# Kernel tuning notes

Measured on AMD Instinct MI355X. Metric: run time of the kernel, lower is better.

Reference implementation:

```python
import jax, jax.numpy as jnp
import numpy as np

N, E, D, H, C = 50000, 1600000, 128, 2, 32

def setup_inputs() -> dict:
    key = jax.random.key(0)
    ks = jax.random.split(key, 8)
    x = jax.random.normal(ks[0], (N, D), jnp.float32)
    edge_index = jax.random.randint(ks[1], (2, E), 0, N)
    intra_enrichment_weights = jax.random.uniform(ks[2], (E,), jnp.float32)
    W = jax.random.normal(ks[3], (D, H * C), jnp.float32) * (1.0 / np.sqrt(D))
    att_src = jax.random.normal(ks[4], (H, C), jnp.float32) * 0.1
    att_dst = jax.random.normal(ks[5], (H, C), jnp.float32) * 0.1
    bias = jnp.zeros((H * C,), jnp.float32)
    enrichment_scale = jnp.asarray(0.01, jnp.float32)
    return dict(x=x, edge_index=edge_index,
                intra_enrichment_weights=intra_enrichment_weights,
                W=W, att_src=att_src, att_dst=att_dst, bias=bias,
                enrichment_scale=enrichment_scale)

def reference(x, edge_index, intra_enrichment_weights, W, att_src, att_dst, bias, enrichment_scale):
    n = x.shape[0]
    xf = jax.nn.elu(x)                       # F.elu on input features
    h = (xf @ W).reshape(n, H, C)            # [N, heads, out]
    # GATConv default add_self_loops=True
    loop = jnp.arange(n, dtype=edge_index.dtype)
    src = jnp.concatenate([edge_index[0], loop])
    dst = jnp.concatenate([edge_index[1], loop])
    a_src = jnp.einsum('nhc,hc->nh', h, att_src)   # [N, H]
    a_dst = jnp.einsum('nhc,hc->nh', h, att_dst)
    alpha = jax.nn.leaky_relu(a_src[src] + a_dst[dst], 0.2)  # [E+N, H]
    # softmax over incoming edges per destination node
    m = jax.ops.segment_max(alpha, dst, num_segments=n)
    e = jnp.exp(alpha - m[dst])
    denom = jax.ops.segment_sum(e, dst, num_segments=n)
    p = e / denom[dst]                       # every node has a self-loop -> denom > 0
    out = jax.ops.segment_sum(h[src] * p[:, :, None], dst, num_segments=n)  # [N, H, C]
    out = out.reshape(n, H * C) + bias
    # enrichment bias (scatter-mean of per-edge weights over source nodes)
    s0 = edge_index[0]
    nw = jax.ops.segment_sum(intra_enrichment_weights, s0, num_segments=n)
    cnt = jax.ops.segment_sum(jnp.ones_like(intra_enrichment_weights), s0, num_segments=n)
    nw = nw / jnp.maximum(cnt, 1.0)
    nw = jnp.clip(nw, 0.2, 5.0)
    scale_factor = 0.1 * jax.nn.sigmoid(enrichment_scale)
    return out + scale_factor * (nw[:, None] - 1.0)
```

## Files before the change

kernel.cpp:

```cpp
#include <hip/hip_runtime.h>


typedef unsigned int u32;
typedef unsigned short u16;

#define SLOTS 4864
#define NB_MAX 400
#define EPB 4096

#define XS 136
#define CS 68

typedef __attribute__((ext_vector_type(8))) short short8;
typedef __attribute__((ext_vector_type(4))) float float4v;

__device__ __forceinline__ u16 f2bf(float f) {
    union { float f; u32 u; } v; v.f = f;
    u32 r = v.u + 0x7fffu + ((v.u >> 16) & 1u);
    return (u16)(r >> 16);
}
__device__ __forceinline__ float bf2f(u16 u) {
    union { u32 i; float f; } v; v.i = ((u32)u) << 16; return v.f;
}
__device__ __forceinline__ float bf_lo(u32 u) {
    union { u32 i; float f; } v; v.i = u << 16; return v.f;
}
__device__ __forceinline__ float bf_hi(u32 u) {
    union { u32 i; float f; } v; v.i = u & 0xFFFF0000u; return v.f;
}
__device__ __forceinline__ void bf_split(float v, short& hi, short& lo) {
    u16 h = f2bf(v);
    float hf = bf2f(h);
    hi = (short)h;
    lo = (short)f2bf(v - hf);
}

__global__ void k_prep(const float* __restrict__ Wm,
                       short* __restrict__ Whf, short* __restrict__ Wlf,
                       int* cursA, int* cursB)
{
    int t = threadIdx.x;
    for (int i = t; i < NB_MAX; i += 256) { cursA[i] = 0; cursB[i] = 0; }
    for (int p = t; p < 1024; p += 256) {
        int frag = p >> 6, l = p & 63;
        int ks = frag >> 2, nt = frag & 3;
        int q = l >> 4, m = l & 15;
        int f = nt * 16 + m;
#pragma unroll
        for (int j = 0; j < 8; ++j) {
            int k = ks * 32 + q * 8 + j;
            float wv = Wm[k * 64 + f];
            short hi, lo; bf_split(wv, hi, lo);
            Whf[p * 8 + j] = hi;
            Wlf[p * 8 + j] = lo;
        }
    }
}

__global__ __launch_bounds__(256) void k_node(
    const float* __restrict__ x,
    const short* __restrict__ Whf, const short* __restrict__ Wlf,
    const float* __restrict__ att_s, const float* __restrict__ att_d,
    u32* __restrict__ hb32, float* __restrict__ a_src, float* __restrict__ a_dst,
    int nN)
{
    __shared__ __align__(16) short Ah[64 * XS];
    __shared__ __align__(16) short Al[64 * XS];
    float* Cl = (float*)Ah;

    int t = threadIdx.x;
    int n0 = blockIdx.x * 64;

    for (int j = 0; j < 8; ++j) {
        int idx = t + 256 * j;
        int r = idx >> 5, c4 = idx & 31;
        int gn = n0 + r;
        float4 xv = make_float4(0.f, 0.f, 0.f, 0.f);
        if (gn < nN) xv = ((const float4*)x)[(size_t)gn * 32 + c4];
        float e[4];
        e[0] = xv.x > 0.f ? xv.x : __expf(xv.x) - 1.f;
        e[1] = xv.y > 0.f ? xv.y : __expf(xv.y) - 1.f;
        e[2] = xv.z > 0.f ? xv.z : __expf(xv.z) - 1.f;
        e[3] = xv.w > 0.f ? xv.w : __expf(xv.w) - 1.f;
        short h4[4], l4[4];
#pragma unroll
        for (int i = 0; i < 4; ++i) bf_split(e[i], h4[i], l4[i]);
        *(short4*)&Ah[r * XS + c4 * 4] = make_short4(h4[0], h4[1], h4[2], h4[3]);
        *(short4*)&Al[r * XS + c4 * 4] = make_short4(l4[0], l4[1], l4[2], l4[3]);
    }
    __syncthreads();

    {
        int w = t >> 6, l = t & 63;
        int q = l >> 4, m = l & 15;
        int arow = w * 16 + m;
        float4v acc[4] = {};
#pragma unroll
        for (int ks = 0; ks < 4; ++ks) {
            int k0 = ks * 32 + q * 8;
            short8 ah = *(const short8*)&Ah[arow * XS + k0];
            short8 al = *(const short8*)&Al[arow * XS + k0];
#pragma unroll
            for (int nt = 0; nt < 4; ++nt) {
                short8 bh = *(const short8*)&Whf[((ks * 4 + nt) * 64 + l) * 8];
                short8 bl = *(const short8*)&Wlf[((ks * 4 + nt) * 64 + l) * 8];
                acc[nt] = __builtin_amdgcn_mfma_f32_16x16x32_bf16(ah, bh, acc[nt], 0, 0, 0);
                acc[nt] = __builtin_amdgcn_mfma_f32_16x16x32_bf16(ah, bl, acc[nt], 0, 0, 0);
                acc[nt] = __builtin_amdgcn_mfma_f32_16x16x32_bf16(al, bh, acc[nt], 0, 0, 0);
            }
        }
        __syncthreads();
#pragma unroll
        for (int nt = 0; nt < 4; ++nt)
#pragma unroll
            for (int r = 0; r < 4; ++r)
                Cl[(w * 16 + q * 4 + r) * CS + nt * 16 + m] = acc[nt][r];
    }
    __syncthreads();

    {
        int nl = t >> 2, fq = t & 3;
        int gn = n0 + nl;
        float ps = 0.f, pd = 0.f;
        if (gn < nN) {
            float hv[16];
#pragma unroll
            for (int i = 0; i < 16; ++i) {
                int f = fq * 16 + i;
                hv[i] = Cl[nl * CS + f];
                ps = fmaf(hv[i], att_s[f], ps);
                pd = fmaf(hv[i], att_d[f], pd);
            }
#pragma unroll
            for (int i = 0; i < 8; ++i) {
                u32 pk = ((u32)f2bf(hv[2 * i + 1]) << 16) | (u32)f2bf(hv[2 * i]);
                hb32[(size_t)gn * 32 + fq * 8 + i] = pk;
            }
        }
        float ps2 = ps + __shfl_xor(ps, 1, 64);
        float pd2 = pd + __shfl_xor(pd, 1, 64);
        if (gn < nN && (fq & 1) == 0) {
            a_src[2 * gn + (fq >> 1)] = ps2;
            a_dst[2 * gn + (fq >> 1)] = pd2;
        }
    }
}

__global__ __launch_bounds__(256) void k_partA(
    const int* __restrict__ ei, const float* __restrict__ wgt,
    int* cursA, int* cursB, u32* bufA, u32* bufB, int E, int nb)
{
    __shared__ u32 arrA[EPB], arrB[EPB];
    __shared__ int cntA[NB_MAX], cntB[NB_MAX];
    __shared__ int lofsA[NB_MAX], lofsB[NB_MAX];
    __shared__ int basA[NB_MAX], basB[NB_MAX];
    __shared__ int part[256];

    int t = threadIdx.x;
    for (int b = t; b < nb; b += 256) { cntA[b] = 0; cntB[b] = 0; }
    __syncthreads();

    int base = blockIdx.x * EPB;
    int nv = min(EPB, E - base);
    int sv[16], dv[16]; float wv[16];
#pragma unroll
    for (int k = 0; k < 16; ++k) {
        int e = base + k * 256 + t;
        if (e < E) { sv[k] = ei[e]; dv[k] = ei[E + e]; wv[k] = wgt[e]; }
        else       { sv[k] = -1;    dv[k] = -1;        wv[k] = 0.f; }
    }
#pragma unroll
    for (int k = 0; k < 16; ++k) {
        if (dv[k] >= 0) {
            atomicAdd(&cntA[dv[k] >> 7], 1);
            atomicAdd(&cntB[sv[k] >> 7], 1);
        }
    }
    __syncthreads();
    for (int b = t; b < nb; b += 256) {
        int ca = cntA[b], cb = cntB[b];
        if (ca > 0) basA[b] = atomicAdd(&cursA[b], ca);
        if (cb > 0) basB[b] = atomicAdd(&cursB[b], cb);
    }
    __syncthreads();
    {
        int b0 = 2 * t, b1 = 2 * t + 1;
        int c0 = (b0 < nb) ? cntA[b0] : 0;
        int c1 = (b1 < nb) ? cntA[b1] : 0;
        part[t] = c0 + c1;
        __syncthreads();
        for (int off = 1; off < 256; off <<= 1) {
            int v = (t >= off) ? part[t - off] : 0;
            __syncthreads();
            part[t] += v;
            __syncthreads();
        }
        int excl = part[t] - (c0 + c1);
        if (b0 < nb) lofsA[b0] = excl;
        if (b1 < nb) lofsA[b1] = excl + c0;
        __syncthreads();
        c0 = (b0 < nb) ? cntB[b0] : 0;
        c1 = (b1 < nb) ? cntB[b1] : 0;
        part[t] = c0 + c1;
        __syncthreads();
        for (int off = 1; off < 256; off <<= 1) {
            int v = (t >= off) ? part[t - off] : 0;
            __syncthreads();
            part[t] += v;
            __syncthreads();
        }
        excl = part[t] - (c0 + c1);
        if (b0 < nb) lofsB[b0] = excl;
        if (b1 < nb) lofsB[b1] = excl + c0;
    }
    __syncthreads();
    for (int b = t; b < nb; b += 256) { cntA[b] = 0; cntB[b] = 0; }
    __syncthreads();
#pragma unroll
    for (int k = 0; k < 16; ++k) {
        if (dv[k] >= 0) {
            int bA = dv[k] >> 7;
            int r = lofsA[bA] + atomicAdd(&cntA[bA], 1);
            arrA[r] = ((u32)bA << 23) | ((u32)(dv[k] & 127) << 16) | (u32)sv[k];
            int bB = sv[k] >> 7;
            u32 wf = (u32)(wv[k] * 65536.f);
            if (wf > 0xFFFFu) wf = 0xFFFFu;
            int r2 = lofsB[bB] + atomicAdd(&cntB[bB], 1);
            arrB[r2] = ((u32)sv[k] << 16) | wf;
        }
    }
    __syncthreads();
    for (int i = t; i < nv; i += 256) {
        u32 va = arrA[i];
        int bA = va >> 23;
        int g = basA[bA] + (i - lofsA[bA]);
        if (g < SLOTS) bufA[bA * SLOTS + g] = va & 0x7FFFFFu;
        u32 vb = arrB[i];
        int bB = vb >> 23;
        int g2 = basB[bB] + (i - lofsB[bB]);
        if (g2 < SLOTS) bufB[bB * SLOTS + g2] = vb & 0x7FFFFFu;
    }
}

__global__ __launch_bounds__(1024) void k_final(
    const u32* __restrict__ hb32,
    const float* __restrict__ a_src, const float* __restrict__ a_dst,
    const u32* __restrict__ bufA, const int* __restrict__ cursA,
    const u32* __restrict__ bufB, const int* __restrict__ cursB,
    const float* __restrict__ bias, const float* __restrict__ esc,
    float* __restrict__ out, int nN)
{
    __shared__ u32 st[SLOTS];
    __shared__ u16 st2[SLOTS];
    __shared__ int ldeg[128], lscan[128], lcur[128];
    __shared__ u32 usum[128];
    __shared__ int ucnt[128];

    int b = blockIdx.x, t = threadIdx.x;
    int n0 = b << 7;
    int nA = cursA[b]; if (nA > SLOTS) nA = SLOTS;
    int nB = cursB[b]; if (nB > SLOTS) nB = SLOTS;

    if (t < 128) { ldeg[t] = 0; lcur[t] = 0; usum[t] = 0; ucnt[t] = 0; }
    __syncthreads();
    for (int i = t; i < nA; i += 1024) {
        u32 v = bufA[(size_t)b * SLOTS + i];
        st[i] = v;
        atomicAdd(&ldeg[v >> 16], 1);
    }
    for (int i = t; i < nB; i += 1024) {
        u32 v = bufB[(size_t)b * SLOTS + i];
        atomicAdd(&usum[v >> 16], v & 0xFFFFu);
        atomicAdd(&ucnt[v >> 16], 1);
    }
    __syncthreads();
    if (t < 128) lscan[t] = ldeg[t];
    __syncthreads();
    for (int off = 1; off < 128; off <<= 1) {
        int v = 0;
        if (t < 128 && t >= off) v = lscan[t - off];
        __syncthreads();
        if (t < 128) lscan[t] += v;
        __syncthreads();
    }
    if (t < 128) lscan[t] -= ldeg[t];
    __syncthreads();
    for (int i = t; i < nA; i += 1024) {
        u32 v = st[i];
        int dl = v >> 16;
        int pos = lscan[dl] + atomicAdd(&lcur[dl], 1);
        st2[pos] = (u16)(v & 0xFFFFu);
    }
    __syncthreads();

    int ws = t >> 6, lane = t & 63;
    int q = lane >> 4, fl = lane & 15, head = fl >> 3;
    const uint2* hb2 = (const uint2*)hb32;
    float escv = esc[0];
    float sf = 0.1f / (1.f + __expf(-escv));
    float4 bb = ((const float4*)bias)[fl];

    for (int dl = ws; dl < 128; dl += 16) {
        int gn = n0 + dl;
        if (gn >= nN) break;
        int beg = lscan[dl], cnt = ldeg[dl];
        float2 adv = ((const float2*)a_dst)[gn];
        float2 asv = ((const float2*)a_src)[gn];
        float t0 = asv.x + adv.x; t0 = t0 > 0.f ? t0 : 0.2f * t0;
        float t1 = asv.y + adv.y; t1 = t1 > 0.f ? t1 : 0.2f * t1;
        float es0 = __expf(t0), es1 = __expf(t1);
        float eself = head ? es1 : es0;

        float acc0 = 0.f, acc1 = 0.f, acc2 = 0.f, acc3 = 0.f;
        if (q == 0) {
            uint2 hs = hb2[(size_t)gn * 16 + fl];
            acc0 = eself * bf_lo(hs.x);
            acc1 = eself * bf_hi(hs.x);
            acc2 = eself * bf_lo(hs.y);
            acc3 = eself * bf_hi(hs.y);
        }
        float dsum0 = 0.f, dsum1 = 0.f;

        int iters = (cnt + 3) >> 2;
#pragma unroll 4
        for (int k = 0; k < iters; ++k) {
            int e = 4 * k + q;
            if (e < cnt) {
                u32 si = st2[beg + e];
                float2 ap = ((const float2*)a_src)[si];
                float v0 = ap.x + adv.x; v0 = v0 > 0.f ? v0 : 0.2f * v0;
                float v1 = ap.y + adv.y; v1 = v1 > 0.f ? v1 : 0.2f * v1;
                float e0 = __expf(v0), e1 = __expf(v1);
                dsum0 += e0; dsum1 += e1;
                uint2 hv = hb2[(size_t)si * 16 + fl];
                float w = head ? e1 : e0;
                acc0 = fmaf(w, bf_lo(hv.x), acc0);
                acc1 = fmaf(w, bf_hi(hv.x), acc1);
                acc2 = fmaf(w, bf_lo(hv.y), acc2);
                acc3 = fmaf(w, bf_hi(hv.y), acc3);
            }
        }
        dsum0 += __shfl_xor(dsum0, 16, 64); dsum0 += __shfl_xor(dsum0, 32, 64);
        dsum1 += __shfl_xor(dsum1, 16, 64); dsum1 += __shfl_xor(dsum1, 32, 64);
        acc0 += __shfl_xor(acc0, 16, 64); acc0 += __shfl_xor(acc0, 32, 64);
        acc1 += __shfl_xor(acc1, 16, 64); acc1 += __shfl_xor(acc1, 32, 64);
        acc2 += __shfl_xor(acc2, 16, 64); acc2 += __shfl_xor(acc2, 32, 64);
        acc3 += __shfl_xor(acc3, 16, 64); acc3 += __shfl_xor(acc3, 32, 64);

        if (q == 0) {
            float den = (head ? es1 : es0) + (head ? dsum1 : dsum0);
            float inv = 1.f / den;
            float cntf = (float)ucnt[dl];
            float nw = ((float)usum[dl] * (1.f / 65536.f)) / fmaxf(cntf, 1.f);
            nw = fminf(fmaxf(nw, 0.2f), 5.f);
            float en = sf * (nw - 1.f);
            float4 o;
            o.x = acc0 * inv + bb.x + en;
            o.y = acc1 * inv + bb.y + en;
            o.z = acc2 * inv + bb.z + en;
            o.w = acc3 * inv + bb.w + en;
            ((float4*)out)[(size_t)gn * 16 + fl] = o;
        }
    }
}

extern "C" void kernel_launch(void* const* d_in, const int* in_sizes, int n_in,
                              void* d_out, int out_size, void* d_ws, size_t ws_size,
                              hipStream_t stream)
{
    const float* x     = (const float*)d_in[0];
    const int*   ei    = (const int*)d_in[1];
    const float* wgt   = (const float*)d_in[2];
    const float* Wm    = (const float*)d_in[3];
    const float* att_s = (const float*)d_in[4];
    const float* att_d = (const float*)d_in[5];
    const float* bias  = (const float*)d_in[6];
    const float* esc   = (const float*)d_in[7];
    float* out = (float*)d_out;

    int nN = in_sizes[0] / 128;
    int E  = in_sizes[2];
    int NB = (nN + 127) / 128;

    char* p = (char*)d_ws;
    auto alloc = [&](size_t bytes) -> char* {
        char* r = p; p += (bytes + 255) & ~(size_t)255; return r;
    };
    u32*   hb32  = (u32*)  alloc((size_t)nN * 32 * 4);
    float* a_src = (float*)alloc((size_t)nN * 2 * 4);
    float* a_dst = (float*)alloc((size_t)nN * 2 * 4);
    short* Whf   = (short*)alloc(16 * 64 * 8 * 2);
    short* Wlf   = (short*)alloc(16 * 64 * 8 * 2);
    int*   cursA = (int*)  alloc(NB_MAX * 4);
    int*   cursB = (int*)  alloc(NB_MAX * 4);
    u32*   bufA  = (u32*)  alloc((size_t)NB * SLOTS * 4);
    u32*   bufB  = (u32*)  alloc((size_t)NB * SLOTS * 4);

    int nblkA = (E + EPB - 1) / EPB;
    int nblkN = (nN + 63) / 64;

    k_prep<<<dim3(1), dim3(256), 0, stream>>>(Wm, Whf, Wlf, cursA, cursB);
    k_node<<<dim3(nblkN), dim3(256), 0, stream>>>(x, Whf, Wlf, att_s, att_d,
                                                  hb32, a_src, a_dst, nN);
    k_partA<<<dim3(nblkA), dim3(256), 0, stream>>>(ei, wgt, cursA, cursB, bufA, bufB, E, NB);
    k_final<<<dim3(NB), dim3(1024), 0, stream>>>(hb32, a_src, a_dst, bufA, cursA,
                                                 bufB, cursB, bias, esc, out, nN);
}
```

Before: 186.7 us.

## Fuse node-transform and edge-partition kernels, lane-parallel edge softmax in final

```diff
diff --git a/kernel.cpp b/kernel.cpp
--- a/kernel.cpp
+++ b/kernel.cpp
@@ -10,6 +10,8 @@
 
 #define XS 136
 #define CS 68
+
+#define SMEM_F 43392
 
 typedef __attribute__((ext_vector_type(8))) short short8;
 typedef __attribute__((ext_vector_type(4))) float float4v;
@@ -57,19 +59,20 @@
     }
 }
 
-__global__ __launch_bounds__(256) void k_node(
+static __device__ __forceinline__ void node_body(
+    char* smem, int nb_id,
     const float* __restrict__ x,
     const short* __restrict__ Whf, const short* __restrict__ Wlf,
     const float* __restrict__ att_s, const float* __restrict__ att_d,
     u32* __restrict__ hb32, float* __restrict__ a_src, float* __restrict__ a_dst,
     int nN)
 {
-    __shared__ __align__(16) short Ah[64 * XS];
-    __shared__ __align__(16) short Al[64 * XS];
+    short* Ah = (short*)smem;
+    short* Al = (short*)(smem + 17408);
     float* Cl = (float*)Ah;
 
     int t = threadIdx.x;
-    int n0 = blockIdx.x * 64;
+    int n0 = nb_id * 64;
 
     for (int j = 0; j < 8; ++j) {
         int idx = t + 256 * j;
@@ -146,21 +149,26 @@
     }
 }
 
-__global__ __launch_bounds__(256) void k_partA(
+static __device__ __forceinline__ void partA_body(
+    char* smem, int pa_id,
     const int* __restrict__ ei, const float* __restrict__ wgt,
     int* cursA, int* cursB, u32* bufA, u32* bufB, int E, int nb)
 {
-    __shared__ u32 arrA[EPB], arrB[EPB];
-    __shared__ int cntA[NB_MAX], cntB[NB_MAX];
-    __shared__ int lofsA[NB_MAX], lofsB[NB_MAX];
-    __shared__ int basA[NB_MAX], basB[NB_MAX];
-    __shared__ int part[256];
+    u32* arrA  = (u32*)smem;
+    u32* arrB  = (u32*)(smem + 16384);
+    int* cntA  = (int*)(smem + 32768);
+    int* cntB  = (int*)(smem + 34368);
+    int* lofsA = (int*)(smem + 35968);
+    int* lofsB = (int*)(smem + 37568);
+    int* basA  = (int*)(smem + 39168);
+    int* basB  = (int*)(smem + 40768);
+    int* part  = (int*)(smem + 42368);
 
     int t = threadIdx.x;
     for (int b = t; b < nb; b += 256) { cntA[b] = 0; cntB[b] = 0; }
     __syncthreads();
 
-    int base = blockIdx.x * EPB;
+    int base = pa_id * EPB;
     int nv = min(EPB, E - base);
     int sv[16], dv[16]; float wv[16];
 #pragma unroll
@@ -226,7 +234,7 @@
             u32 wf = (u32)(wv[k] * 65536.f);
             if (wf > 0xFFFFu) wf = 0xFFFFu;
             int r2 = lofsB[bB] + atomicAdd(&cntB[bB], 1);
-            arrB[r2] = ((u32)sv[k] << 16) | wf;
+            arrB[r2] = ((u32)bB << 23) | ((u32)(sv[k] & 127) << 16) | wf;
         }
     }
     __syncthreads();
@@ -242,6 +250,27 @@
     }
 }
 
+__global__ __launch_bounds__(256) void k_fused(
+    const float* __restrict__ x,
+    const short* __restrict__ Whf, const short* __restrict__ Wlf,
+    const float* __restrict__ att_s, const float* __restrict__ att_d,
+    u32* __restrict__ hb32, float* __restrict__ a_src, float* __restrict__ a_dst,
+    const int* __restrict__ ei, const float* __restrict__ wgt,
+    int* cursA, int* cursB, u32* bufA, u32* bufB,
+    int E, int nb, int nblkA, int nN)
+{
+    __shared__ __align__(16) char smem[SMEM_F];
+    int bid = blockIdx.x;
+    int q3 = bid / 3;
+    if ((bid % 3) == 0 && q3 < nblkA) {
+        partA_body(smem, q3, ei, wgt, cursA, cursB, bufA, bufB, E, nb);
+    } else {
+        int npa_before = min(q3 + ((bid % 3) ? 1 : 0), nblkA);
+        node_body(smem, bid - npa_before, x, Whf, Wlf, att_s, att_d,
+                  hb32, a_src, a_dst, nN);
+    }
+}
+
 __global__ __launch_bounds__(1024) void k_final(
     const u32* __restrict__ hb32,
     const float* __restrict__ a_src, const float* __restrict__ a_dst,
@@ -309,10 +338,10 @@
         float t0 = asv.x + adv.x; t0 = t0 > 0.f ? t0 : 0.2f * t0;
         float t1 = asv.y + adv.y; t1 = t1 > 0.f ? t1 : 0.2f * t1;
         float es0 = __expf(t0), es1 = __expf(t1);
-        float eself = head ? es1 : es0;
 
         float acc0 = 0.f, acc1 = 0.f, acc2 = 0.f, acc3 = 0.f;
         if (q == 0) {
+            float eself = head ? es1 : es0;
             uint2 hs = hb2[(size_t)gn * 16 + fl];
             acc0 = eself * bf_lo(hs.x);
             acc1 = eself * bf_hi(hs.x);
@@ -321,27 +350,38 @@
         }
         float dsum0 = 0.f, dsum1 = 0.f;
 
-        int iters = (cnt + 3) >> 2;
-#pragma unroll 4
-        for (int k = 0; k < iters; ++k) {
-            int e = 4 * k + q;
-            if (e < cnt) {
-                u32 si = st2[beg + e];
+        for (int b0 = 0; b0 < cnt; b0 += 64) {
+            int wn = cnt - b0; if (wn > 64) wn = 64;
+            u32 si = (u32)gn; float e0 = 0.f, e1 = 0.f;
+            if (lane < wn) {
+                si = (u32)st2[beg + b0 + lane];
                 float2 ap = ((const float2*)a_src)[si];
                 float v0 = ap.x + adv.x; v0 = v0 > 0.f ? v0 : 0.2f * v0;
                 float v1 = ap.y + adv.y; v1 = v1 > 0.f ? v1 : 0.2f * v1;
-                float e0 = __expf(v0), e1 = __expf(v1);
-                dsum0 += e0; dsum1 += e1;
-                uint2 hv = hb2[(size_t)si * 16 + fl];
-                float w = head ? e1 : e0;
+                e0 = __expf(v0); e1 = __expf(v1);
+            }
+            dsum0 += e0; dsum1 += e1;
+
+            int iters = (wn + 3) >> 2;
+#pragma unroll 8
+            for (int k = 0; k < iters; ++k) {
+                int e = 4 * k + q;
+                u32 rsi = __shfl(si, e, 64);
+                uint2 hv = hb2[(size_t)rsi * 16 + fl];
+                float w0 = __shfl(e0, e, 64);
+                float w1 = __shfl(e1, e, 64);
+                float w = head ? w1 : w0;
                 acc0 = fmaf(w, bf_lo(hv.x), acc0);
                 acc1 = fmaf(w, bf_hi(hv.x), acc1);
                 acc2 = fmaf(w, bf_lo(hv.y), acc2);
                 acc3 = fmaf(w, bf_hi(hv.y), acc3);
             }
         }
-        dsum0 += __shfl_xor(dsum0, 16, 64); dsum0 += __shfl_xor(dsum0, 32, 64);
-        dsum1 += __shfl_xor(dsum1, 16, 64); dsum1 += __shfl_xor(dsum1, 32, 64);
+#pragma unroll
+        for (int off = 1; off < 64; off <<= 1) {
+            dsum0 += __shfl_xor(dsum0, off, 64);
+            dsum1 += __shfl_xor(dsum1, off, 64);
+        }
         acc0 += __shfl_xor(acc0, 16, 64); acc0 += __shfl_xor(acc0, 32, 64);
         acc1 += __shfl_xor(acc1, 16, 64); acc1 += __shfl_xor(acc1, 32, 64);
         acc2 += __shfl_xor(acc2, 16, 64); acc2 += __shfl_xor(acc2, 32, 64);
@@ -398,11 +438,13 @@
 
     int nblkA = (E + EPB - 1) / EPB;
     int nblkN = (nN + 63) / 64;
+    int nblkF = nblkA + nblkN;
 
     k_prep<<<dim3(1), dim3(256), 0, stream>>>(Wm, Whf, Wlf, cursA, cursB);
-    k_node<<<dim3(nblkN), dim3(256), 0, stream>>>(x, Whf, Wlf, att_s, att_d,
-                                                  hb32, a_src, a_dst, nN);
-    k_partA<<<dim3(nblkA), dim3(256), 0, stream>>>(ei, wgt, cursA, cursB, bufA, bufB, E, NB);
+    k_fused<<<dim3(nblkF), dim3(256), 0, stream>>>(x, Whf, Wlf, att_s, att_d,
+                                                   hb32, a_src, a_dst,
+                                                   ei, wgt, cursA, cursB, bufA, bufB,
+                                                   E, NB, nblkA, nN);
     k_final<<<dim3(NB), dim3(1024), 0, stream>>>(hb32, a_src, a_dst, bufA, cursA,
                                                  bufB, cursB, bias, esc, out, nN);
 }
```

Result: faster. 178.5 us (-4.4%).
